# Kernel tuning notes

Measured on AMD Instinct MI355X. Metric: run time of the kernel, lower is better.

The kernel has to match this reference:

```python
import jax, jax.numpy as jnp
import numpy as np

K = 3        # dcn filter size
STRIDE = 2
PAD = 1
NEG_SLOPE = 0.1


def conv2d(x, w, stride, pad):
    return jax.lax.conv_general_dilated(
        x, w, (stride, stride), [(pad, pad), (pad, pad)],
        dimension_numbers=('NCHW', 'OIHW', 'NCHW'))


def setup_inputs() -> dict:
    key = jax.random.key(0)
    ks = jax.random.split(key, 6)
    N, H, W = 8, 256, 256
    return {
        'input_tensor': jax.random.normal(ks[0], (N, 3, H, W), jnp.float32),
        'conv1_w': jax.random.normal(ks[1], (8, 3, 1, 1), jnp.float32) * 0.3,
        'conv1_b': jax.random.normal(ks[2], (8,), jnp.float32) * 0.1,
        'offset_w': jax.random.normal(ks[3], (3 * K * K, 8, K, K), jnp.float32) * 0.05,
        'offset_b': jax.random.normal(ks[4], (3 * K * K,), jnp.float32) * 0.05,
        'dcn_w': jax.random.normal(ks[5], (512, 8, K, K), jnp.float32) * 0.1,
    }


def _dcnv2(x, offset_w, offset_b, dcn_w):
    # Modulated deformable conv v2 (bias_attr=False).
    N, C, H, W = x.shape
    K2 = K * K
    om = conv2d(x, offset_w, STRIDE, PAD) + offset_b[None, :, None, None]  # [N,3K2,Ho,Wo]
    offset = om[:, :2 * K2]
    mask = jax.nn.sigmoid(om[:, 2 * K2:])                                  # [N,K2,Ho,Wo]
    Ho, Wo = mask.shape[2], mask.shape[3]
    off = offset.reshape(N, K2, 2, Ho, Wo)  # (dy, dx) per kernel point
    dy, dx = off[:, :, 0], off[:, :, 1]
    ky, kx = jnp.meshgrid(jnp.arange(K), jnp.arange(K), indexing='ij')
    base_y = (jnp.arange(Ho) * STRIDE - PAD).astype(x.dtype)
    base_x = (jnp.arange(Wo) * STRIDE - PAD).astype(x.dtype)
    # Fractional sampling positions in input coordinates: [N,K2,Ho,Wo]
    py = base_y[None, None, :, None] + ky.reshape(-1)[None, :, None, None] + dy
    px = base_x[None, None, None, :] + kx.reshape(-1)[None, :, None, None] + dx
    # Bilinear sampling with zero padding outside the image.
    y0 = jnp.floor(py)
    x0 = jnp.floor(px)
    n_idx = jnp.arange(N)[:, None, None, None]
    cols = jnp.zeros((N, K2, Ho, Wo, C), x.dtype)
    for oy in (0.0, 1.0):
        for ox in (0.0, 1.0):
            yy = y0 + oy
            xx = x0 + ox
            w = (1.0 - jnp.abs(py - yy)) * (1.0 - jnp.abs(px - xx))
            valid = (yy >= 0) & (yy < H) & (xx >= 0) & (xx < W)
            iy = jnp.clip(yy, 0, H - 1).astype(jnp.int32)
            ix = jnp.clip(xx, 0, W - 1).astype(jnp.int32)
            # x[n_idx, :, iy, ix] -> [N,K2,Ho,Wo,C]
            cols = cols + jnp.where(valid, w, 0.0)[..., None] * x[n_idx, :, iy, ix]
    cols = cols * mask[..., None]  # modulation
    out_c = dcn_w.shape[0]
    return jnp.einsum('nkhwc,ock->nohw', cols, dcn_w.reshape(out_c, C, K2))


def reference(input_tensor, conv1_w, conv1_b, offset_w, offset_b, dcn_w):
    y = conv2d(input_tensor, conv1_w, 1, 0) + conv1_b[None, :, None, None]
    y = jnp.where(y >= 0, y, NEG_SLOPE * y)  # LeakyReLU(0.1)
    return _dcnv2(y, offset_w, offset_b, dcn_w)
```

## Files before the change

### kernel.cpp

```cpp
#include <hip/hip_runtime.h>
#include <math.h>

#define NB   8
#define HH   256
#define WW   256
#define CY   8
#define HO   128
#define WO   128
#define OCN  512
#define K2   9
#define KJ   72
#define KP   104

typedef short bf16x8 __attribute__((ext_vector_type(8)));
typedef float f32x4  __attribute__((ext_vector_type(4)));

static __device__ inline unsigned short f2bf(float f) {
    union { float f; unsigned u; } v; v.f = f;
    unsigned r = (v.u + 0x7FFFu + ((v.u >> 16) & 1u)) >> 16;
    return (unsigned short)r;
}

__global__ __launch_bounds__(256) void k_conv1(const float* __restrict__ x,
                                               const float* __restrict__ w,
                                               const float* __restrict__ b,
                                               float* __restrict__ y) {
    int idx = blockIdx.x * 256 + threadIdx.x;
    int n = idx >> 16, hw = idx & 65535;
    const float* xp = x + (size_t)n * 3 * 65536 + hw;
    float x0 = xp[0], x1 = xp[65536], x2 = xp[131072];
    float o[8];
#pragma unroll
    for (int oc = 0; oc < 8; ++oc) {
        float v = fmaf(w[oc*3+0], x0, fmaf(w[oc*3+1], x1, fmaf(w[oc*3+2], x2, b[oc])));
        o[oc] = v >= 0.f ? v : 0.1f * v;
    }
    float* yp = y + (size_t)idx * 8;
    *(float4*)(yp + 0) = make_float4(o[0], o[1], o[2], o[3]);
    *(float4*)(yp + 4) = make_float4(o[4], o[5], o[6], o[7]);
}

__global__ __launch_bounds__(256) void k_wpad(const float* __restrict__ wd,
                                              unsigned short* __restrict__ wdb) {
    int i = blockIdx.x * 256 + threadIdx.x;
    int row = i / KP;
    int k = i - row * KP;
    float v = (k < KJ) ? wd[row * KJ + k] : 0.f;
    wdb[i] = f2bf(v);
}

__global__ __launch_bounds__(512, 4) void k_fused(const float* __restrict__ y,
                                                  const float* __restrict__ ow,
                                                  const float* __restrict__ ob,
                                                  const unsigned short* __restrict__ wdb,
                                                  float* __restrict__ out) {
    __shared__ __align__(16) unsigned short cT[128 * KP];

    int t = threadIdx.x;
    int pix0 = blockIdx.x * 128;
    int nimg = pix0 >> 14;
    int ho   = (pix0 & 16383) >> 7;
    const float* yn = y + (size_t)nimg * (HH * WW * CY);

    if (t < 128) {
        int wo = t;
        float acc[27];
#pragma unroll
        for (int oc = 0; oc < 27; ++oc) acc[oc] = ob[oc];

#pragma unroll 1
        for (int pos = 0; pos < 9; ++pos) {
            int kh = pos / 3, kw = pos - kh * 3;
            int hi = 2 * ho - 1 + kh, wi = 2 * wo - 1 + kw;
            float4 a  = make_float4(0.f, 0.f, 0.f, 0.f);
            float4 c4 = make_float4(0.f, 0.f, 0.f, 0.f);
            if ((unsigned)hi < 256u && (unsigned)wi < 256u) {
                const float* yp = yn + ((size_t)hi * 256 + wi) * 8;
                a  = *(const float4*)(yp + 0);
                c4 = *(const float4*)(yp + 4);
            }
            const float* wp = ow + pos;
#pragma unroll
            for (int oc = 0; oc < 27; ++oc) {
                float s = fmaf(wp[oc*72 + 0*9], a.x,
                          fmaf(wp[oc*72 + 1*9], a.y,
                          fmaf(wp[oc*72 + 2*9], a.z,
                          fmaf(wp[oc*72 + 3*9], a.w,
                          fmaf(wp[oc*72 + 4*9], c4.x,
                          fmaf(wp[oc*72 + 5*9], c4.y,
                          fmaf(wp[oc*72 + 6*9], c4.z,
                               wp[oc*72 + 7*9] * c4.w)))))));
                acc[oc] += s;
            }
        }

#pragma unroll
        for (int k = 0; k < 9; ++k) {
            float dy = acc[2 * k], dx = acc[2 * k + 1];
            float m  = 1.f / (1.f + expf(-acc[18 + k]));
            float py = (float)(2 * ho - 1 + (k / 3)) + dy;
            float px = (float)(2 * wo - 1 + (k % 3)) + dx;
            float y0f = floorf(py), x0f = floorf(px);
            float fy = py - y0f, fx = px - x0f;
            int y0 = (int)y0f, x0 = (int)x0f;
            float s0=0,s1=0,s2=0,s3=0,s4=0,s5=0,s6=0,s7=0;
#pragma unroll
            for (int oy = 0; oy < 2; ++oy) {
#pragma unroll
                for (int ox = 0; ox < 2; ++ox) {
                    int yy = y0 + oy, xx = x0 + ox;
                    float wgt = (oy ? fy : 1.f - fy) * (ox ? fx : 1.f - fx);
                    if ((unsigned)yy < 256u && (unsigned)xx < 256u) {
                        const float* yp = yn + ((size_t)yy * 256 + xx) * 8;
                        float4 a  = *(const float4*)(yp + 0);
                        float4 c4 = *(const float4*)(yp + 4);
                        s0 = fmaf(wgt, a.x,  s0); s1 = fmaf(wgt, a.y,  s1);
                        s2 = fmaf(wgt, a.z,  s2); s3 = fmaf(wgt, a.w,  s3);
                        s4 = fmaf(wgt, c4.x, s4); s5 = fmaf(wgt, c4.y, s5);
                        s6 = fmaf(wgt, c4.z, s6); s7 = fmaf(wgt, c4.w, s7);
                    }
                }
            }
            unsigned short* cp = cT + t * KP + k;
            cp[0*9] = f2bf(m*s0); cp[1*9] = f2bf(m*s1); cp[2*9] = f2bf(m*s2); cp[3*9] = f2bf(m*s3);
            cp[4*9] = f2bf(m*s4); cp[5*9] = f2bf(m*s5); cp[6*9] = f2bf(m*s6); cp[7*9] = f2bf(m*s7);
        }
        {
            uint4 z; z.x = z.y = z.z = z.w = 0u;
            uint4* zp = (uint4*)((unsigned char*)cT + (size_t)t * 2 * KP + 144);
            zp[0] = z; zp[1] = z; zp[2] = z; zp[3] = z;
        }
    }
    __syncthreads();

    int wave = t >> 6, lane = t & 63, lr = lane & 15, lk = lane >> 4;
    int hwbase = pix0 & 16383;
#pragma unroll
    for (int p = 0; p < 2; ++p) {
        int ocb = p * 256 + wave * 32;
        bf16x8 aF[2][3];
#pragma unroll
        for (int m = 0; m < 2; ++m)
#pragma unroll
            for (int kk = 0; kk < 3; ++kk)
                aF[m][kk] = *(const bf16x8*)(wdb + (size_t)(ocb + m * 16 + lr) * KP + kk * 32 + lk * 8);

        f32x4 acc2[2][8];
#pragma unroll
        for (int m = 0; m < 2; ++m)
#pragma unroll
            for (int n = 0; n < 8; ++n) acc2[m][n] = (f32x4){0.f, 0.f, 0.f, 0.f};

#pragma unroll
        for (int kk = 0; kk < 3; ++kk) {
#pragma unroll
            for (int n = 0; n < 8; ++n) {
                bf16x8 bF = *(const bf16x8*)(cT + (n * 16 + lr) * KP + kk * 32 + lk * 8);
                acc2[0][n] = __builtin_amdgcn_mfma_f32_16x16x32_bf16(aF[0][kk], bF, acc2[0][n], 0, 0, 0);
                acc2[1][n] = __builtin_amdgcn_mfma_f32_16x16x32_bf16(aF[1][kk], bF, acc2[1][n], 0, 0, 0);
            }
        }

#pragma unroll
        for (int m = 0; m < 2; ++m) {
            int oc = ocb + m * 16 + lk * 4;
#pragma unroll
            for (int n = 0; n < 8; ++n) {
                int hw = hwbase + n * 16 + lr;
                float* op = out + ((size_t)nimg * OCN + oc) * 16384 + hw;
                __builtin_nontemporal_store(acc2[m][n][0], op);
                __builtin_nontemporal_store(acc2[m][n][1], op + 16384);
                __builtin_nontemporal_store(acc2[m][n][2], op + 2 * 16384);
                __builtin_nontemporal_store(acc2[m][n][3], op + 3 * 16384);
            }
        }
    }
}

extern "C" void kernel_launch(void* const* d_in, const int* in_sizes, int n_in,
                              void* d_out, int out_size, void* d_ws, size_t ws_size,
                              hipStream_t stream) {
    const float* x   = (const float*)d_in[0];
    const float* c1w = (const float*)d_in[1];
    const float* c1b = (const float*)d_in[2];
    const float* ow  = (const float*)d_in[3];
    const float* ob  = (const float*)d_in[4];
    const float* dw  = (const float*)d_in[5];
    float* out = (float*)d_out;

    float* yb = (float*)d_ws;
    unsigned short* wdb = (unsigned short*)((unsigned char*)d_ws + 16777216);

    hipLaunchKernelGGL(k_conv1, dim3(2048), dim3(256), 0, stream, x, c1w, c1b, yb);
    hipLaunchKernelGGL(k_wpad, dim3(208), dim3(256), 0, stream, dw, wdb);
    hipLaunchKernelGGL(k_fused, dim3(1024), dim3(512), 0, stream, yb, ow, ob, wdb, out);
}
```

Baseline: 340.2 us.

## Spread offset conv and bilinear sampling across all 512 threads

The offset/mask convolution and the deformable sampling, which before ran only on 128 of 512 threads, are now split across all threads. Each quarter of the block computes 7 (or 6) of the 27 offset channels, and the results go into a new shared-memory buffer. After a barrier, the 1152 (pixel, kernel-point) sampling tasks are spread over all threads. This cuts the serial per-thread prologue before the MFMA stage, at the cost of extra shared memory, one more barrier, and redundant input loads for the offset conv in each thread group.

```diff
diff --git a/kernel.cpp b/kernel.cpp
--- a/kernel.cpp
+++ b/kernel.cpp
@@ -54,6 +54,7 @@
                                                   const float* __restrict__ ob,
                                                   const unsigned short* __restrict__ wdb,
                                                   float* __restrict__ out) {
+    __shared__ float om[128][27];
     __shared__ __align__(16) unsigned short cT[128 * KP];
 
     int t = threadIdx.x;
@@ -63,10 +64,18 @@
     const float* yn = y + (size_t)nimg * (HH * WW * CY);
 
     if (t < 128) {
-        int wo = t;
-        float acc[27];
-#pragma unroll
-        for (int oc = 0; oc < 27; ++oc) acc[oc] = ob[oc];
+        uint4 z; z.x = z.y = z.z = z.w = 0u;
+        uint4* zp = (uint4*)((unsigned char*)cT + (size_t)t * 2 * KP + 144);
+        zp[0] = z; zp[1] = z; zp[2] = z; zp[3] = z;
+    }
+
+    {
+        int wo = t & 127, q = t >> 7;
+        int oc0 = q * 7;
+        int noc = (q == 3) ? 6 : 7;
+        float accL[7];
+#pragma unroll
+        for (int j = 0; j < 7; ++j) accL[j] = (j < noc) ? ob[oc0 + j] : 0.f;
 
 #pragma unroll 1
         for (int pos = 0; pos < 9; ++pos) {
@@ -81,25 +90,36 @@
             }
             const float* wp = ow + pos;
 #pragma unroll
-            for (int oc = 0; oc < 27; ++oc) {
-                float s = fmaf(wp[oc*72 + 0*9], a.x,
-                          fmaf(wp[oc*72 + 1*9], a.y,
-                          fmaf(wp[oc*72 + 2*9], a.z,
-                          fmaf(wp[oc*72 + 3*9], a.w,
-                          fmaf(wp[oc*72 + 4*9], c4.x,
-                          fmaf(wp[oc*72 + 5*9], c4.y,
-                          fmaf(wp[oc*72 + 6*9], c4.z,
-                               wp[oc*72 + 7*9] * c4.w)))))));
-                acc[oc] += s;
-            }
-        }
-
-#pragma unroll
-        for (int k = 0; k < 9; ++k) {
-            float dy = acc[2 * k], dx = acc[2 * k + 1];
-            float m  = 1.f / (1.f + expf(-acc[18 + k]));
-            float py = (float)(2 * ho - 1 + (k / 3)) + dy;
-            float px = (float)(2 * wo - 1 + (k % 3)) + dx;
+            for (int j = 0; j < 7; ++j) {
+                if (j < noc) {
+                    int oc = oc0 + j;
+                    float s = fmaf(wp[oc*72 + 0*9], a.x,
+                              fmaf(wp[oc*72 + 1*9], a.y,
+                              fmaf(wp[oc*72 + 2*9], a.z,
+                              fmaf(wp[oc*72 + 3*9], a.w,
+                              fmaf(wp[oc*72 + 4*9], c4.x,
+                              fmaf(wp[oc*72 + 5*9], c4.y,
+                              fmaf(wp[oc*72 + 6*9], c4.z,
+                                   wp[oc*72 + 7*9] * c4.w)))))));
+                    accL[j] += s;
+                }
+            }
+        }
+#pragma unroll
+        for (int j = 0; j < 7; ++j)
+            if (j < noc) om[wo][oc0 + j] = accL[j];
+    }
+    __syncthreads();
+
+#pragma unroll
+    for (int base = 0; base < 1152; base += 512) {
+        int it = base + t;
+        if (it < 1152) {
+            int spx = it & 127, k = it >> 7;
+            float dy = om[spx][2 * k], dx = om[spx][2 * k + 1];
+            float m  = 1.f / (1.f + expf(-om[spx][18 + k]));
+            float py = (float)(2 * ho  - 1 + (k / 3)) + dy;
+            float px = (float)(2 * spx - 1 + (k % 3)) + dx;
             float y0f = floorf(py), x0f = floorf(px);
             float fy = py - y0f, fx = px - x0f;
             int y0 = (int)y0f, x0 = (int)x0f;
@@ -121,14 +141,9 @@
                     }
                 }
             }
-            unsigned short* cp = cT + t * KP + k;
+            unsigned short* cp = cT + spx * KP + k;
             cp[0*9] = f2bf(m*s0); cp[1*9] = f2bf(m*s1); cp[2*9] = f2bf(m*s2); cp[3*9] = f2bf(m*s3);
             cp[4*9] = f2bf(m*s4); cp[5*9] = f2bf(m*s5); cp[6*9] = f2bf(m*s6); cp[7*9] = f2bf(m*s7);
-        }
-        {
-            uint4 z; z.x = z.y = z.z = z.w = 0u;
-            uint4* zp = (uint4*)((unsigned char*)cT + (size_t)t * 2 * KP + 144);
-            zp[0] = z; zp[1] = z; zp[2] = z; zp[3] = z;
         }
     }
     __syncthreads();
```

After: 342.0 us. Within noise of the previous version (+0.5%).
